# Performance work log

Measured on AMD Instinct MI355X. Metric: run time of the kernel, lower is better.

Reference implementation:

```python
import jax, jax.numpy as jnp
import numpy as np

B, FNP, D = 16, 4096, 512
P, S, F = 16, 8, 32

def setup_inputs() -> dict:
    key = jax.random.key(0)
    k1, k2 = jax.random.split(key)
    token_states = jax.random.normal(k1, (B, FNP, D), dtype=jnp.float32)
    W = jax.random.normal(k2, (2 * P, D), dtype=jnp.float32) * 0.02
    b = jnp.zeros((2 * P,), dtype=jnp.float32)
    return {"token_states": token_states, "W": W, "b": b, "T": 1032}

def reference(token_states, W, b, T):
    Bsz, FNp, Dm = token_states.shape
    Np = FNp // F
    h = token_states.reshape(Bsz, F, Np, Dm)
    # per-patch linear head: [B, F, Np, 2P]
    raw = jnp.einsum('bfnd,ed->bfne', h, W) + b
    raw = raw.reshape(Bsz, F, Np, 2, P)
    mu = raw[:, :, :, 0, :]                                   # [B, F, Np, P]
    sigma = jnp.clip(jnp.exp(raw[:, :, :, 1, :]), 1e-06, None)
    mu = jnp.transpose(mu, (0, 2, 3, 1))                      # [B, Np, P, F]
    sigma = jnp.transpose(sigma, (0, 2, 3, 1))
    # overlap-add fold: time index for each (patch, offset)
    t = (jnp.arange(Np)[:, None] * S + jnp.arange(P)[None, :]).reshape(-1)  # [Np*P]
    valid = (t < T)
    t_c = jnp.where(valid, t, 0)
    vmask = valid.astype(mu.dtype)[None, :, None]             # [1, Np*P, 1]
    mu_flat = mu.reshape(Bsz, Np * P, F) * vmask
    sg_flat = sigma.reshape(Bsz, Np * P, F) * vmask
    mu_full = jnp.zeros((Bsz, T, F), dtype=mu.dtype).at[:, t_c, :].add(mu_flat)
    sigma_full = jnp.zeros((Bsz, T, F), dtype=mu.dtype).at[:, t_c, :].add(sg_flat)
    counts = jnp.zeros((T,), dtype=mu.dtype).at[t_c].add(valid.astype(mu.dtype))
    counts = jnp.clip(counts, 1.0, None)[None, :, None]       # [1, T, 1]
    return (mu_full / counts, sigma_full / counts)
```

## Files before the change

### kernel.cpp

```cpp
#include <hip/hip_runtime.h>
#include <math.h>

#define B_    16
#define F_    32
#define NP_   128
#define D_    512
#define P_    16
#define KC    64
#define NCH   8
#define BUFW  (NP_ * KC)
#define NRING 4
#define EOFF  (NRING * BUFW)

typedef __attribute__((ext_vector_type(8)))  short  short8;
typedef __attribute__((ext_vector_type(16))) float  floatx16;

union Frag { short8 v; unsigned int u[4]; };

__device__ inline unsigned int cvt_pk_bf16(float lo, float hi) {
    unsigned int r;
    asm volatile("v_cvt_pk_bf16_f32 %0, %1, %2" : "=v"(r) : "v"(lo), "v"(hi));
    return r;
}

#define EBAR asm volatile("s_waitcnt lgkmcnt(0)\n\ts_barrier" ::: "memory")

__global__ __launch_bounds__(512, 2)
void pd_kernel(const float* __restrict__ ts,
               const float* __restrict__ W,
               const float* __restrict__ bias,
               float* __restrict__ out, int T)
{
    __shared__ float smem[EOFF + NP_ * 33];

    const int tid  = threadIdx.x;
    const int lane = tid & 63;
    const int wave = tid >> 6;
    const int mt   = wave & 3;
    const int p    = wave >> 2;

    const int d  = blockIdx.x;
    const int b  = (d & 7) | (((d >> 7) & 1) << 3);
    const int fp = (d >> 3) & 15;
    const float* __restrict__ tsb0 = ts + ((size_t)(b * F_ + 2 * fp) * NP_) * D_;
    const float* __restrict__ tsb1 = tsb0 + (size_t)NP_ * D_;

    auto STAGE = [&](const float* base, int cc) {
#pragma unroll
        for (int it = 0; it < 4; ++it) {
            const int slot = it * 512 + tid;
            const int r2 = slot >> 4;
            const int qg = (slot & 15) ^ (r2 & 15);
            const float* src = base + r2 * D_ + cc * KC + (qg << 2);
            float* dst = smem + (cc & 3) * BUFW + (slot << 2);
            __builtin_amdgcn_global_load_lds(
                (const __attribute__((address_space(1))) unsigned int*)src,
                (__attribute__((address_space(3))) unsigned int*)dst,
                16, 0, 0);
        }
    };

    STAGE(tsb0, 0);
    STAGE(tsb0, 1);
    __builtin_amdgcn_sched_barrier(0);

    const int e_b = lane & 31;
    const int kh  = lane >> 5;
    Frag bf[NCH][2];
    {
        const float* wb = W + (size_t)e_b * D_ + kh * 8;
#pragma unroll
        for (int c = 0; c < NCH; ++c)
#pragma unroll
            for (int j = 0; j < 2; ++j) {
                const int k = (4 * c + p + 2 * j) * 16;
                const float4 lo = *(const float4*)(wb + k);
                const float4 hi = *(const float4*)(wb + k + 4);
                bf[c][j].u[0] = cvt_pk_bf16(lo.x, lo.y);
                bf[c][j].u[1] = cvt_pk_bf16(lo.z, lo.w);
                bf[c][j].u[2] = cvt_pk_bf16(hi.x, hi.y);
                bf[c][j].u[3] = cvt_pk_bf16(hi.z, hi.w);
            }
    }
    __builtin_amdgcn_sched_barrier(0);

    STAGE(tsb0, 2);
    __builtin_amdgcn_sched_barrier(0);

    const int ldsrow = mt * 32 + (lane & 31);
    const int sw16   = ldsrow & 15;
    const int aq     = p * 4 + kh * 2;

    const int TF = T * F_;
    const size_t halfoff = (size_t)B_ * TF;
    float* const E = smem + EOFF;

    auto COMPUTE = [&](int c, floatx16& acc) {
        const float* rowp = smem + (c & 3) * BUFW + ldsrow * KC;
#pragma unroll
        for (int j = 0; j < 2; ++j) {
            const int q0 = aq + j * 8;
            const float4 lo = *(const float4*)(rowp + ((q0 ^ sw16) << 2));
            const float4 hi = *(const float4*)(rowp + (((q0 + 1) ^ sw16) << 2));
            Frag a;
            a.u[0] = cvt_pk_bf16(lo.x, lo.y);
            a.u[1] = cvt_pk_bf16(lo.z, lo.w);
            a.u[2] = cvt_pk_bf16(hi.x, hi.y);
            a.u[3] = cvt_pk_bf16(hi.z, hi.w);
            acc = __builtin_amdgcn_mfma_f32_32x32x16_bf16(a.v, bf[c][j].v, acc, 0, 0, 0);
        }
    };

    floatx16 accA, accB;
#pragma unroll
    for (int r = 0; r < 16; ++r) { accA[r] = 0.f; accB[r] = 0.f; }

#pragma unroll
    for (int c = 0; c < NCH; ++c) {
        asm volatile("s_waitcnt vmcnt(8)\n\ts_barrier" ::: "memory");
        __builtin_amdgcn_sched_barrier(0);
        if (c <= 4) STAGE(tsb0, c + 3);
        else        STAGE(tsb1, c - 5);
        __builtin_amdgcn_sched_barrier(0);
        COMPUTE(c, accA);
    }

    const int f0 = 2 * fp;
    const int QT = (2 * T + 3) / 4;
#pragma unroll
    for (int c = 0; c < NCH; ++c) {
        if (c <= 4)
            asm volatile("s_waitcnt vmcnt(8) lgkmcnt(0)\n\ts_barrier" ::: "memory");
        else if (c == 5)
            asm volatile("s_waitcnt vmcnt(8) lgkmcnt(0)\n\ts_barrier" ::: "memory");
        else if (c == 6)
            asm volatile("s_waitcnt vmcnt(4) lgkmcnt(0)\n\ts_barrier" ::: "memory");
        else
            asm volatile("s_waitcnt vmcnt(0) lgkmcnt(0)\n\ts_barrier" ::: "memory");
        __builtin_amdgcn_sched_barrier(0);

        if (c <= 4) STAGE(tsb1, c + 3);
        __builtin_amdgcn_sched_barrier(0);

        if (c == 0) {
            if (p == 0) {
#pragma unroll
                for (int r = 0; r < 16; ++r) {
                    const int rowl = (r & 3) + 8 * (r >> 2) + 4 * kh;
                    E[(mt * 32 + rowl) * 33 + e_b] = accA[r];
                }
            }
        } else if (c == 1) {
            if (p == 1) {
#pragma unroll
                for (int r = 0; r < 16; ++r) {
                    const int rowl = (r & 3) + 8 * (r >> 2) + 4 * kh;
                    float v = E[(mt * 32 + rowl) * 33 + e_b] + accA[r] + bias[e_b];
                    if (e_b >= P_) v = fmaxf(expf(v), 1e-6f);
                    E[(mt * 32 + rowl) * 33 + e_b] = v;
                }
            }
        } else if (c >= 2 && c <= 5) {
            const int g  = c - 2;
            const int hi = min((g + 1) * QT, 2 * T);
            for (int item = g * QT + tid; item < hi; item += 512) {
                const int half = (item >= T) ? 1 : 0;
                const int t    = item - half * T;
                const int nmax = min(NP_ - 1, t >> 3);
                const int nmin = (t > 8) ? ((t - 8) >> 3) : 0;
                float sum = 0.f;
                const int cnt = nmax - nmin + 1;
                for (int nn = nmin; nn <= nmax; ++nn)
                    sum += E[nn * 33 + (half << 4) + (t - (nn << 3))];
                const float r = (cnt > 0) ? sum / (float)cnt : 0.f;
                out[(size_t)half * halfoff + (size_t)b * TF + (size_t)t * F_ + f0] = r;
            }
        }

        COMPUTE(c, accB);
    }

    const int f1 = 2 * fp + 1;
    if (p == 0) {
#pragma unroll
        for (int r = 0; r < 16; ++r) {
            const int rowl = (r & 3) + 8 * (r >> 2) + 4 * kh;
            E[(mt * 32 + rowl) * 33 + e_b] = accB[r];
        }
    }
    EBAR;
    if (p == 1) {
#pragma unroll
        for (int r = 0; r < 16; ++r) {
            const int rowl = (r & 3) + 8 * (r >> 2) + 4 * kh;
            float v = E[(mt * 32 + rowl) * 33 + e_b] + accB[r] + bias[e_b];
            if (e_b >= P_) v = fmaxf(expf(v), 1e-6f);
            E[(mt * 32 + rowl) * 33 + e_b] = v;
        }
    }
    EBAR;
    for (int item = tid; item < 2 * T; item += 512) {
        const int half = (item >= T) ? 1 : 0;
        const int t    = item - half * T;
        const int nmax = min(NP_ - 1, t >> 3);
        const int nmin = (t > 8) ? ((t - 8) >> 3) : 0;
        float sum = 0.f;
        const int cnt = nmax - nmin + 1;
        for (int nn = nmin; nn <= nmax; ++nn)
            sum += E[nn * 33 + (half << 4) + (t - (nn << 3))];
        const float r = (cnt > 0) ? sum / (float)cnt : 0.f;
        out[(size_t)half * halfoff + (size_t)b * TF + (size_t)t * F_ + f1] = r;
    }
}

extern "C" void kernel_launch(void* const* d_in, const int* in_sizes, int n_in,
                              void* d_out, int out_size, void* d_ws, size_t ws_size,
                              hipStream_t stream)
{
    const float* ts   = (const float*)d_in[0];
    const float* W    = (const float*)d_in[1];
    const float* bias = (const float*)d_in[2];
    float* out = (float*)d_out;

    const int T = out_size / (2 * B_ * F_);

    dim3 grid(B_ * F_ / 2);
    dim3 block(512);
    pd_kernel<<<grid, block, 0, stream>>>(ts, W, bias, out, T);
}
```

Before: 36.69 us.

## Stage activations through registers, convert to bf16 before LDS, single 16-chunk pipeline

Replaces the direct global-to-LDS async copies of fp32 activations with register-staged loads (3-deep register ring). Each chunk is converted to bf16 once, then written to a 4-slot LDS ring with an XOR swizzle. The two 8-chunk loops become one 16-chunk loop that writes chunk g+1 and loads chunk g+3 before a barrier. This halves LDS footprint and read traffic and removes redundant per-wave conversion in the compute step, at the cost of many more VGPRs for staging, which may pressure occupancy at 512 threads with 2 blocks/CU. It also adds a barrier per chunk where the write-after-read ordering on the ring must hold.

```diff
diff --git a/kernel.cpp b/kernel.cpp
--- a/kernel.cpp
+++ b/kernel.cpp
@@ -7,10 +7,9 @@
 #define D_    512
 #define P_    16
 #define KC    64
-#define NCH   8
-#define BUFW  (NP_ * KC)
-#define NRING 4
-#define EOFF  (NRING * BUFW)
+#define NCHT  16
+#define SLOTF 4096
+#define EOFFF (4 * SLOTF)
 
 typedef __attribute__((ext_vector_type(8)))  short  short8;
 typedef __attribute__((ext_vector_type(16))) float  floatx16;
@@ -23,7 +22,8 @@
     return r;
 }
 
-#define EBAR asm volatile("s_waitcnt lgkmcnt(0)\n\ts_barrier" ::: "memory")
+#define SB  __builtin_amdgcn_sched_barrier(0)
+#define BAR asm volatile("s_waitcnt lgkmcnt(0)\n\ts_barrier" ::: "memory")
 
 __global__ __launch_bounds__(512, 2)
 void pd_kernel(const float* __restrict__ ts,
@@ -31,7 +31,7 @@
                const float* __restrict__ bias,
                float* __restrict__ out, int T)
 {
-    __shared__ float smem[EOFF + NP_ * 33];
+    __shared__ float smem[EOFFF + NP_ * 33];
 
     const int tid  = threadIdx.x;
     const int lane = tid & 63;
@@ -45,32 +45,40 @@
     const float* __restrict__ tsb0 = ts + ((size_t)(b * F_ + 2 * fp) * NP_) * D_;
     const float* __restrict__ tsb1 = tsb0 + (size_t)NP_ * D_;
 
-    auto STAGE = [&](const float* base, int cc) {
-#pragma unroll
-        for (int it = 0; it < 4; ++it) {
-            const int slot = it * 512 + tid;
-            const int r2 = slot >> 4;
-            const int qg = (slot & 15) ^ (r2 & 15);
-            const float* src = base + r2 * D_ + cc * KC + (qg << 2);
-            float* dst = smem + (cc & 3) * BUFW + (slot << 2);
-            __builtin_amdgcn_global_load_lds(
-                (const __attribute__((address_space(1))) unsigned int*)src,
-                (__attribute__((address_space(3))) unsigned int*)dst,
-                16, 0, 0);
-        }
+    const int lr = tid >> 2;
+    const int lu = tid & 3;
+
+    float4 st[3][4];
+    auto LOAD = [&](int g) {
+        const float* src = (g < 8 ? tsb0 : tsb1)
+                         + (size_t)lr * D_ + (g & 7) * KC + lu * 16;
+#pragma unroll
+        for (int i = 0; i < 4; ++i) st[g % 3][i] = ((const float4*)src)[i];
     };
-
-    STAGE(tsb0, 0);
-    STAGE(tsb0, 1);
-    __builtin_amdgcn_sched_barrier(0);
+    auto WRITE = [&](int g) {
+        Frag q0, q1;
+        q0.u[0] = cvt_pk_bf16(st[g%3][0].x, st[g%3][0].y);
+        q0.u[1] = cvt_pk_bf16(st[g%3][0].z, st[g%3][0].w);
+        q0.u[2] = cvt_pk_bf16(st[g%3][1].x, st[g%3][1].y);
+        q0.u[3] = cvt_pk_bf16(st[g%3][1].z, st[g%3][1].w);
+        q1.u[0] = cvt_pk_bf16(st[g%3][2].x, st[g%3][2].y);
+        q1.u[1] = cvt_pk_bf16(st[g%3][2].z, st[g%3][2].w);
+        q1.u[2] = cvt_pk_bf16(st[g%3][3].x, st[g%3][3].y);
+        q1.u[3] = cvt_pk_bf16(st[g%3][3].z, st[g%3][3].w);
+        short8* slot = (short8*)(smem + (g & 3) * SLOTF);
+        slot[lr * 8 + ((2 * lu)     ^ (lr & 7))] = q0.v;
+        slot[lr * 8 + ((2 * lu + 1) ^ (lr & 7))] = q1.v;
+    };
 
     const int e_b = lane & 31;
     const int kh  = lane >> 5;
-    Frag bf[NCH][2];
+    Frag bf[8][2];
+    LOAD(0); SB;
+    LOAD(1); LOAD(2); SB;
     {
         const float* wb = W + (size_t)e_b * D_ + kh * 8;
 #pragma unroll
-        for (int c = 0; c < NCH; ++c)
+        for (int c = 0; c < 8; ++c)
 #pragma unroll
             for (int j = 0; j < 2; ++j) {
                 const int k = (4 * c + p + 2 * j) * 16;
@@ -82,67 +90,41 @@
                 bf[c][j].u[3] = cvt_pk_bf16(hi.z, hi.w);
             }
     }
-    __builtin_amdgcn_sched_barrier(0);
-
-    STAGE(tsb0, 2);
-    __builtin_amdgcn_sched_barrier(0);
-
-    const int ldsrow = mt * 32 + (lane & 31);
-    const int sw16   = ldsrow & 15;
-    const int aq     = p * 4 + kh * 2;
+    SB;
+    WRITE(0);
+    BAR; SB;
+
+    const int ro = mt * 32 + (lane & 31);
+
+    auto COMPUTE = [&](int g, floatx16& acc) {
+        const short8* slot = (const short8*)(smem + (g & 3) * SLOTF);
+#pragma unroll
+        for (int j = 0; j < 2; ++j) {
+            const int qq = (p + 2 * j) * 2 + kh;
+            Frag a; a.v = slot[ro * 8 + (qq ^ (ro & 7))];
+            acc = __builtin_amdgcn_mfma_f32_32x32x16_bf16(a.v, bf[g & 7][j].v, acc, 0, 0, 0);
+        }
+    };
+
+    floatx16 accA, accB;
+#pragma unroll
+    for (int r = 0; r < 16; ++r) { accA[r] = 0.f; accB[r] = 0.f; }
 
     const int TF = T * F_;
     const size_t halfoff = (size_t)B_ * TF;
-    float* const E = smem + EOFF;
-
-    auto COMPUTE = [&](int c, floatx16& acc) {
-        const float* rowp = smem + (c & 3) * BUFW + ldsrow * KC;
-#pragma unroll
-        for (int j = 0; j < 2; ++j) {
-            const int q0 = aq + j * 8;
-            const float4 lo = *(const float4*)(rowp + ((q0 ^ sw16) << 2));
-            const float4 hi = *(const float4*)(rowp + (((q0 + 1) ^ sw16) << 2));
-            Frag a;
-            a.u[0] = cvt_pk_bf16(lo.x, lo.y);
-            a.u[1] = cvt_pk_bf16(lo.z, lo.w);
-            a.u[2] = cvt_pk_bf16(hi.x, hi.y);
-            a.u[3] = cvt_pk_bf16(hi.z, hi.w);
-            acc = __builtin_amdgcn_mfma_f32_32x32x16_bf16(a.v, bf[c][j].v, acc, 0, 0, 0);
-        }
-    };
-
-    floatx16 accA, accB;
-#pragma unroll
-    for (int r = 0; r < 16; ++r) { accA[r] = 0.f; accB[r] = 0.f; }
-
-#pragma unroll
-    for (int c = 0; c < NCH; ++c) {
-        asm volatile("s_waitcnt vmcnt(8)\n\ts_barrier" ::: "memory");
-        __builtin_amdgcn_sched_barrier(0);
-        if (c <= 4) STAGE(tsb0, c + 3);
-        else        STAGE(tsb1, c - 5);
-        __builtin_amdgcn_sched_barrier(0);
-        COMPUTE(c, accA);
-    }
-
+    float* const E = smem + EOFFF;
     const int f0 = 2 * fp;
     const int QT = (2 * T + 3) / 4;
-#pragma unroll
-    for (int c = 0; c < NCH; ++c) {
-        if (c <= 4)
-            asm volatile("s_waitcnt vmcnt(8) lgkmcnt(0)\n\ts_barrier" ::: "memory");
-        else if (c == 5)
-            asm volatile("s_waitcnt vmcnt(8) lgkmcnt(0)\n\ts_barrier" ::: "memory");
-        else if (c == 6)
-            asm volatile("s_waitcnt vmcnt(4) lgkmcnt(0)\n\ts_barrier" ::: "memory");
-        else
-            asm volatile("s_waitcnt vmcnt(0) lgkmcnt(0)\n\ts_barrier" ::: "memory");
-        __builtin_amdgcn_sched_barrier(0);
-
-        if (c <= 4) STAGE(tsb1, c + 3);
-        __builtin_amdgcn_sched_barrier(0);
-
-        if (c == 0) {
+
+#pragma unroll
+    for (int g = 0; g < NCHT; ++g) {
+        if (g + 1 < NCHT) WRITE(g + 1);
+        if (g + 3 < NCHT) LOAD(g + 3);
+        SB;
+        BAR;
+        SB;
+
+        if (g == 8) {
             if (p == 0) {
 #pragma unroll
                 for (int r = 0; r < 16; ++r) {
@@ -150,7 +132,7 @@
                     E[(mt * 32 + rowl) * 33 + e_b] = accA[r];
                 }
             }
-        } else if (c == 1) {
+        } else if (g == 9) {
             if (p == 1) {
 #pragma unroll
                 for (int r = 0; r < 16; ++r) {
@@ -160,10 +142,10 @@
                     E[(mt * 32 + rowl) * 33 + e_b] = v;
                 }
             }
-        } else if (c >= 2 && c <= 5) {
-            const int g  = c - 2;
-            const int hi = min((g + 1) * QT, 2 * T);
-            for (int item = g * QT + tid; item < hi; item += 512) {
+        } else if (g >= 10 && g <= 13) {
+            const int gq = g - 10;
+            const int hi = min((gq + 1) * QT, 2 * T);
+            for (int item = gq * QT + tid; item < hi; item += 512) {
                 const int half = (item >= T) ? 1 : 0;
                 const int t    = item - half * T;
                 const int nmax = min(NP_ - 1, t >> 3);
@@ -177,7 +159,8 @@
             }
         }
 
-        COMPUTE(c, accB);
+        if (g < 8) COMPUTE(g, accA);
+        else       COMPUTE(g, accB);
     }
 
     const int f1 = 2 * fp + 1;
@@ -188,7 +171,7 @@
             E[(mt * 32 + rowl) * 33 + e_b] = accB[r];
         }
     }
-    EBAR;
+    BAR;
     if (p == 1) {
 #pragma unroll
         for (int r = 0; r < 16; ++r) {
@@ -198,7 +181,7 @@
             E[(mt * 32 + rowl) * 33 + e_b] = v;
         }
     }
-    EBAR;
+    BAR;
     for (int item = tid; item < 2 * T; item += 512) {
         const int half = (item >= T) ? 1 : 0;
         const int t    = item - half * T;
```

Measured after the change: 36.19 us. No clear change (-1.4%).
